# Kernel optimization log

Measured on AMD Instinct MI355X. Metric: run time of the kernel, lower is better.

## Reference

```python
import jax, jax.numpy as jnp
import numpy as np

HIDDEN = 1280
NUM_HEADS = 20
HEAD_DIM = HIDDEN // NUM_HEADS
B, S = 2, 2048


def setup_inputs() -> dict:
    key = jax.random.key(0)
    k1, k2, k3, k4, k5 = jax.random.split(key, 5)
    scale_in = 1.0 / np.sqrt(HIDDEN)
    return {
        "x": jax.random.normal(k1, (B, S, HIDDEN), dtype=jnp.float32),
        "w_attn": jax.random.normal(k2, (HIDDEN, 3 * HIDDEN), dtype=jnp.float32) * scale_in,
        "b_attn": jax.random.normal(k3, (3 * HIDDEN,), dtype=jnp.float32) * 0.02,
        "w_proj": jax.random.normal(k4, (HIDDEN, HIDDEN), dtype=jnp.float32) * scale_in,
        "b_proj": jax.random.normal(k5, (HIDDEN,), dtype=jnp.float32) * 0.02,
    }


def reference(x, w_attn, b_attn, w_proj, b_proj):
    b, s, _ = x.shape
    scale = 1.0 / np.sqrt(HEAD_DIM)
    qkv = x @ w_attn + b_attn                      # [B,S,3H]
    q, k, v = jnp.split(qkv, 3, axis=-1)

    def heads(t):  # [B,S,H] -> [B,nh,S,hd]
        return t.reshape(b, s, NUM_HEADS, HEAD_DIM).transpose(0, 2, 1, 3)

    q, k, v = heads(q), heads(k), heads(v)
    attn = jnp.einsum("bhqd,bhkd->bhqk", q, k) * scale
    causal = jnp.tril(jnp.ones((s, s), dtype=bool))
    attn = jnp.where(causal, attn, jnp.float32(-jnp.inf))
    attn = jax.nn.softmax(attn, axis=-1)           # dropout = identity (eval)
    out = jnp.einsum("bhqk,bhkd->bhqd", attn, v)
    out = out.transpose(0, 2, 1, 3).reshape(b, s, HIDDEN)
    return out @ w_proj + b_proj
```

## Files before the change

kernel.cpp:

```cpp
#include <hip/hip_runtime.h>

typedef unsigned short u16;
typedef __attribute__((ext_vector_type(8))) short bf16x8;
typedef __attribute__((ext_vector_type(4))) float f32x4;
typedef __attribute__((ext_vector_type(4))) unsigned short u16x4;

#define MFMA16 __builtin_amdgcn_mfma_f32_16x16x32_bf16

__device__ __forceinline__ u16 f2bf(float f) {
  unsigned int u = __float_as_uint(f);
  u += 0x7fff + ((u >> 16) & 1);
  return (u16)(u >> 16);
}

__device__ __forceinline__ float vexp2(float x) {
  float r; asm("v_exp_f32 %0, %1" : "=v"(r) : "v"(x)); return r;
}

template<int CTRL>
__device__ __forceinline__ float dppf(float v) {
  return __int_as_float(__builtin_amdgcn_update_dpp(0, __float_as_int(v), CTRL, 0xF, 0xF, true));
}
__device__ __forceinline__ float rowsum16(float v) {
  v += dppf<0xB1>(v);
  v += dppf<0x4E>(v);
  v += dppf<0x141>(v);
  v += dppf<0x140>(v);
  return v;
}

__device__ __forceinline__ void gload_lds16(const void* g, void* l) {
  __builtin_amdgcn_global_load_lds((__attribute__((address_space(1))) void*)g,
                                   (__attribute__((address_space(3))) void*)l,
                                   16, 0, 0);
}

__global__ void k_cast(const float* __restrict__ src, u16* __restrict__ dst, int n4) {
  int i = blockIdx.x * 256 + threadIdx.x;
  if (i >= n4) return;
  const float4 v = reinterpret_cast<const float4*>(src)[i];
  u16x4 o = {f2bf(v.x), f2bf(v.y), f2bf(v.z), f2bf(v.w)};
  reinterpret_cast<u16x4*>(dst)[i] = o;
}

__global__ void k_transpose_cast(const float* __restrict__ src, u16* __restrict__ dst,
                                 int R, int C) {
  __shared__ float tile[64][65];
  const int t = threadIdx.x;
  const int c0 = blockIdx.x * 64, r0 = blockIdx.y * 64;
#pragma unroll
  for (int i = 0; i < 16; ++i) {
    int e = i * 256 + t;
    int r = e >> 6, c = e & 63;
    tile[r][c] = src[(size_t)(r0 + r) * C + (c0 + c)];
  }
  __syncthreads();
#pragma unroll
  for (int i = 0; i < 16; ++i) {
    int e = i * 256 + t;
    int r = e >> 6, c = e & 63;
    dst[(size_t)(c0 + r) * R + (r0 + c)] = f2bf(tile[c][r]);
  }
}

__global__ __launch_bounds__(256, 2) void k_gemm_qkv(
    const u16* __restrict__ A, const u16* __restrict__ Bt,
    const float* __restrict__ bias,
    u16* __restrict__ qo, u16* __restrict__ ko, u16* __restrict__ vt) {
  constexpr int K = 1280;
  __shared__ u16 Alds[128 * 64];
  __shared__ u16 Blds[128 * 64];
  const int t = threadIdx.x;
  const int lane = t & 63, wave = t >> 6;
  const int wr = wave >> 1, wc = wave & 1;
  const int l15 = lane & 15, lhi = lane >> 4;
  const int m0 = blockIdx.x * 128, n0 = blockIdx.y * 128;

  f32x4 acc[4][4];
#pragma unroll
  for (int mi = 0; mi < 4; ++mi)
#pragma unroll
    for (int ni = 0; ni < 4; ++ni) acc[mi][ni] = f32x4{0.f, 0.f, 0.f, 0.f};

  const int srow = t >> 3;
  const int scol = (t & 7) * 8;
  const u16* Ag = A + (size_t)(m0 + srow) * K + scol;
  const u16* Bg = Bt + (size_t)(n0 + srow) * K + scol;
  char* Al = (char*)Alds + wave * 1024;
  char* Bl = (char*)Blds + wave * 1024;

  for (int k0 = 0; k0 < K; k0 += 64) {
    __syncthreads();
#pragma unroll
    for (int it = 0; it < 4; ++it) {
      gload_lds16(Ag + (it * 32) * K + k0, Al + it * 4096);
      gload_lds16(Bg + (it * 32) * K + k0, Bl + it * 4096);
    }
    asm volatile("s_waitcnt vmcnt(0)" ::: "memory");
    __syncthreads();
    const u16* Ab = Alds + (wr * 64 + l15) * 64 + lhi * 8;
    const u16* Bb = Blds + (wc * 64 + l15) * 64 + lhi * 8;
    bf16x8 af[4][2], bfv[4][2];
#pragma unroll
    for (int x = 0; x < 4; ++x) {
      af[x][0] = *(const bf16x8*)(Ab + x * 1024);
      af[x][1] = *(const bf16x8*)(Ab + x * 1024 + 32);
      bfv[x][0] = *(const bf16x8*)(Bb + x * 1024);
      bfv[x][1] = *(const bf16x8*)(Bb + x * 1024 + 32);
    }
#pragma unroll
    for (int mi = 0; mi < 4; ++mi)
#pragma unroll
      for (int ni = 0; ni < 4; ++ni) {
        acc[mi][ni] = MFMA16(af[mi][0], bfv[ni][0], acc[mi][ni], 0, 0, 0);
        acc[mi][ni] = MFMA16(af[mi][1], bfv[ni][1], acc[mi][ni], 0, 0, 0);
      }
  }

  const int which = n0 >= 2560 ? 2 : (n0 >= 1280 ? 1 : 0);
  const int bbq = m0 >> 11;
  const int sbase = (m0 & 2047) + wr * 64;
  if (which < 2) {
    u16* outp = which == 0 ? qo : ko;
#pragma unroll
    for (int ni = 0; ni < 4; ++ni) {
      const int n_abs = n0 + wc * 64 + ni * 16 + l15;
      const int nn = n_abs - which * 1280;
      const int h = nn >> 6, d = nn & 63;
      const float bv = bias[n_abs];
#pragma unroll
      for (int mi = 0; mi < 4; ++mi) {
#pragma unroll
        for (int i = 0; i < 4; ++i) {
          const int ss = sbase + mi * 16 + lhi * 4 + i;
          outp[(((size_t)(bbq * 20 + h) * 2048 + ss) << 6) + d] = f2bf(acc[mi][ni][i] + bv);
        }
      }
    }
  } else {
#pragma unroll
    for (int ni = 0; ni < 4; ++ni) {
      const int n_abs = n0 + wc * 64 + ni * 16 + l15;
      const int nn = n_abs - 2560;
      const int h = nn >> 6, d = nn & 63;
      const float bv = bias[n_abs];
      u16* vrow = vt + ((size_t)(bbq * 20 + h) * 64 + d) * 2048;
#pragma unroll
      for (int mi = 0; mi < 4; ++mi) {
        const int ss = sbase + mi * 16 + lhi * 4;
        u16x4 pk = {f2bf(acc[mi][ni][0] + bv), f2bf(acc[mi][ni][1] + bv),
                    f2bf(acc[mi][ni][2] + bv), f2bf(acc[mi][ni][3] + bv)};
        *(u16x4*)(vrow + ss) = pk;
      }
    }
  }
}

__global__ __launch_bounds__(256, 2) void k_gemm_proj(
    const u16* __restrict__ A, const u16* __restrict__ Bt,
    const float* __restrict__ bias, float* __restrict__ out) {
  constexpr int K = 1280;
  __shared__ u16 Alds[128 * 64];
  __shared__ u16 Blds[128 * 64];
  const int t = threadIdx.x;
  const int lane = t & 63, wave = t >> 6;
  const int wr = wave >> 1, wc = wave & 1;
  const int l15 = lane & 15, lhi = lane >> 4;
  const int m0 = blockIdx.x * 128, n0 = blockIdx.y * 128;

  f32x4 acc[4][4];
#pragma unroll
  for (int mi = 0; mi < 4; ++mi)
#pragma unroll
    for (int ni = 0; ni < 4; ++ni) acc[mi][ni] = f32x4{0.f, 0.f, 0.f, 0.f};

  const int srow = t >> 3;
  const int scol = (t & 7) * 8;
  const u16* Ag = A + (size_t)(m0 + srow) * K + scol;
  const u16* Bg = Bt + (size_t)(n0 + srow) * K + scol;
  char* Al = (char*)Alds + wave * 1024;
  char* Bl = (char*)Blds + wave * 1024;

  for (int k0 = 0; k0 < K; k0 += 64) {
    __syncthreads();
#pragma unroll
    for (int it = 0; it < 4; ++it) {
      gload_lds16(Ag + (it * 32) * K + k0, Al + it * 4096);
      gload_lds16(Bg + (it * 32) * K + k0, Bl + it * 4096);
    }
    asm volatile("s_waitcnt vmcnt(0)" ::: "memory");
    __syncthreads();
    const u16* Ab = Alds + (wr * 64 + l15) * 64 + lhi * 8;
    const u16* Bb = Blds + (wc * 64 + l15) * 64 + lhi * 8;
    bf16x8 af[4][2], bfv[4][2];
#pragma unroll
    for (int x = 0; x < 4; ++x) {
      af[x][0] = *(const bf16x8*)(Ab + x * 1024);
      af[x][1] = *(const bf16x8*)(Ab + x * 1024 + 32);
      bfv[x][0] = *(const bf16x8*)(Bb + x * 1024);
      bfv[x][1] = *(const bf16x8*)(Bb + x * 1024 + 32);
    }
#pragma unroll
    for (int mi = 0; mi < 4; ++mi)
#pragma unroll
      for (int ni = 0; ni < 4; ++ni) {
        acc[mi][ni] = MFMA16(af[mi][0], bfv[ni][0], acc[mi][ni], 0, 0, 0);
        acc[mi][ni] = MFMA16(af[mi][1], bfv[ni][1], acc[mi][ni], 0, 0, 0);
      }
  }

#pragma unroll
  for (int ni = 0; ni < 4; ++ni) {
    const int n_abs = n0 + wc * 64 + ni * 16 + l15;
    const float bv = bias[n_abs];
#pragma unroll
    for (int mi = 0; mi < 4; ++mi) {
#pragma unroll
      for (int i = 0; i < 4; ++i) {
        const int m_abs = m0 + wr * 64 + mi * 16 + lhi * 4 + i;
        out[(size_t)m_abs * 1280 + n_abs] = acc[mi][ni][i] + bv;
      }
    }
  }
}

__global__ __launch_bounds__(256, 3) void k_attn11(
    const u16* __restrict__ Qg, const u16* __restrict__ Kg,
    const u16* __restrict__ VT, u16* __restrict__ ao) {
  __shared__ __align__(16) char kvs[2][16384];
  __shared__ u16 Plds[4][32 * 72];
  const int t = threadIdx.x;
  const int lane = t & 63, wave = t >> 6;
  const int l15 = lane & 15, lhi = lane >> 4;
  const int bh = blockIdx.x;
  const int qt = 15 - blockIdx.y;
  const int bb = bh / 20, hh = bh % 20;
  const int q0w = qt * 128 + wave * 32;
  const int nkv = 2 * (qt + 1);
  const size_t base = (size_t)bh * 2048 * 64;
  const size_t vtb = (size_t)bh * 64 * 2048;
  u16* Pw = Plds[wave];

  const int sls = (lane & 7) ^ (lane >> 3);
  const int soff0 = ((lhi ^ (lane & 7)) << 4);
  const int soff1 = (((4 + lhi) ^ (lane & 7)) << 4);

  bf16x8 qf[2][2];
#pragma unroll
  for (int mr = 0; mr < 2; ++mr)
#pragma unroll
    for (int kk = 0; kk < 2; ++kk)
      qf[mr][kk] = *(const bf16x8*)(Qg + base + (size_t)(q0w + mr * 16 + l15) * 64 + kk * 32 + lhi * 8);

  f32x4 o[2][4];
  float lp[2][4];
#pragma unroll
  for (int mr = 0; mr < 2; ++mr) {
#pragma unroll
    for (int i = 0; i < 4; ++i) lp[mr][i] = 0.f;
#pragma unroll
    for (int dc = 0; dc < 4; ++dc) o[mr][dc] = f32x4{0.f, 0.f, 0.f, 0.f};
  }
  const float c1 = 0.18033688f;
  const float M = 16.0f;
  const int lastw = (q0w + 31) >> 6;

  auto stage = [&](char* buf, int kv0) {
#pragma unroll
    for (int j = 0; j < 2; ++j) {
      const int r = j * 32 + wave * 8 + (lane >> 3);
      gload_lds16(Kg + base + (size_t)(kv0 + r) * 64 + sls * 8,
                  buf + j * 4096 + wave * 1024);
      gload_lds16(VT + vtb + (size_t)r * 2048 + kv0 + sls * 8,
                  buf + 8192 + j * 4096 + wave * 1024);
    }
  };

  stage(kvs[0], 0);

  for (int tk = 0; tk < nkv; ++tk) {
    const int kv0 = tk * 64;
    if (tk + 1 < nkv) {
      stage(kvs[(tk + 1) & 1], kv0 + 64);
      asm volatile("s_waitcnt vmcnt(4)" ::: "memory");
    } else {
      asm volatile("s_waitcnt vmcnt(0)" ::: "memory");
    }
    __syncthreads();

    if (tk <= lastw) {
      const char* Krow = kvs[tk & 1] + l15 * 128;
      const char* Vrow = kvs[tk & 1] + 8192 + l15 * 128;
      f32x4 sc[2][4];
#pragma unroll
      for (int c = 0; c < 4; ++c) {
        const bf16x8 kf0 = *(const bf16x8*)(Krow + c * 2048 + soff0);
        const bf16x8 kf1 = *(const bf16x8*)(Krow + c * 2048 + soff1);
#pragma unroll
        for (int mr = 0; mr < 2; ++mr) {
          f32x4 z = MFMA16(qf[mr][0], kf0, f32x4{0.f, 0.f, 0.f, 0.f}, 0, 0, 0);
          z = MFMA16(qf[mr][1], kf1, z, 0, 0, 0);
          sc[mr][c] = z;
        }
      }
      if (kv0 + 63 > q0w) {
#pragma unroll
        for (int mr = 0; mr < 2; ++mr)
#pragma unroll
          for (int c = 0; c < 4; ++c)
#pragma unroll
            for (int i = 0; i < 4; ++i) {
              const int qa = q0w + mr * 16 + lhi * 4 + i;
              const int ka = kv0 + c * 16 + l15;
              sc[mr][c][i] = (ka <= qa) ? sc[mr][c][i] : -3.0e38f;
            }
      }
#pragma unroll
      for (int mr = 0; mr < 2; ++mr)
#pragma unroll
        for (int i = 0; i < 4; ++i) {
          float psum = 0.f;
#pragma unroll
          for (int c = 0; c < 4; ++c) {
            const float p = vexp2(__builtin_fmaf(sc[mr][c][i], c1, -M));
            psum += p;
            Pw[(mr * 16 + lhi * 4 + i) * 72 + c * 16 + l15] = (u16)(__float_as_uint(p) >> 16);
          }
          lp[mr][i] += psum;
        }
      bf16x8 pf[2][2];
#pragma unroll
      for (int mr = 0; mr < 2; ++mr)
#pragma unroll
        for (int kk = 0; kk < 2; ++kk)
          pf[mr][kk] = *(const bf16x8*)&Pw[(mr * 16 + l15) * 72 + kk * 32 + lhi * 8];
#pragma unroll
      for (int dc = 0; dc < 4; ++dc) {
        const bf16x8 vf0 = *(const bf16x8*)(Vrow + dc * 2048 + soff0);
        const bf16x8 vf1 = *(const bf16x8*)(Vrow + dc * 2048 + soff1);
#pragma unroll
        for (int mr = 0; mr < 2; ++mr) {
          o[mr][dc] = MFMA16(pf[mr][0], vf0, o[mr][dc], 0, 0, 0);
          o[mr][dc] = MFMA16(pf[mr][1], vf1, o[mr][dc], 0, 0, 0);
        }
      }
    }
    __syncthreads();
  }

#pragma unroll
  for (int mr = 0; mr < 2; ++mr)
#pragma unroll
    for (int i = 0; i < 4; ++i) {
      const float lfull = rowsum16(lp[mr][i]);
      const float inv = 1.0f / lfull;
      const int qa = q0w + mr * 16 + lhi * 4 + i;
#pragma unroll
      for (int dc = 0; dc < 4; ++dc) {
        const int d = dc * 16 + l15;
        ao[((size_t)(bb * 2048 + qa)) * 1280 + hh * 64 + d] = f2bf(o[mr][dc][i] * inv);
      }
    }
}

extern "C" void kernel_launch(void* const* d_in, const int* in_sizes, int n_in,
                              void* d_out, int out_size, void* d_ws, size_t ws_size,
                              hipStream_t stream) {
  (void)in_sizes; (void)n_in; (void)out_size; (void)ws_size;
  const float* x      = (const float*)d_in[0];
  const float* w_attn = (const float*)d_in[1];
  const float* b_attn = (const float*)d_in[2];
  const float* w_proj = (const float*)d_in[3];
  const float* b_proj = (const float*)d_in[4];
  float* out = (float*)d_out;

  char* ws = (char*)d_ws;
  u16* x_bf = (u16*)(ws + 0);
  u16* wa_t = (u16*)(ws + 10485760);
  u16* wp_t = (u16*)(ws + 20316160);
  u16* q_ws = (u16*)(ws + 23592960);
  u16* k_ws = (u16*)(ws + 34078720);
  u16* vt   = (u16*)(ws + 44564480);
  u16* ao   = x_bf;

  k_cast<<<5120, 256, 0, stream>>>(x, x_bf, 4096 * 1280 / 4);
  k_transpose_cast<<<dim3(60, 20), 256, 0, stream>>>(w_attn, wa_t, 1280, 3840);
  k_transpose_cast<<<dim3(20, 20), 256, 0, stream>>>(w_proj, wp_t, 1280, 1280);
  k_gemm_qkv<<<dim3(32, 30), 256, 0, stream>>>(x_bf, wa_t, b_attn, q_ws, k_ws, vt);
  k_attn11<<<dim3(40, 16), 256, 0, stream>>>(q_ws, k_ws, vt, ao);
  k_gemm_proj<<<dim3(32, 10), 256, 0, stream>>>(ao, wp_t, b_proj, out);
}
```

Before: 147.4 us.

## Double-buffer LDS tiles in QKV and projection GEMMs to overlap loads with MFMA

Both GEMM kernels now keep two LDS buffers for the A and B tiles and issue the global-to-LDS loads for the next K step before computing on the current one. This aims to hide global load latency behind the MFMA work and drops one barrier per iteration. LDS use doubles to 64KB per block, which may cut the number of blocks that fit per CU under launch_bounds(256,2). The GEMMs are only part of the total time, since attention dominates.

```diff
diff --git a/kernel.cpp b/kernel.cpp
--- a/kernel.cpp
+++ b/kernel.cpp
@@ -68,8 +68,8 @@
     const float* __restrict__ bias,
     u16* __restrict__ qo, u16* __restrict__ ko, u16* __restrict__ vt) {
   constexpr int K = 1280;
-  __shared__ u16 Alds[128 * 64];
-  __shared__ u16 Blds[128 * 64];
+  __shared__ u16 Alds[2][128 * 64];
+  __shared__ u16 Blds[2][128 * 64];
   const int t = threadIdx.x;
   const int lane = t & 63, wave = t >> 6;
   const int wr = wave >> 1, wc = wave & 1;
@@ -86,20 +86,26 @@
   const int scol = (t & 7) * 8;
   const u16* Ag = A + (size_t)(m0 + srow) * K + scol;
   const u16* Bg = Bt + (size_t)(n0 + srow) * K + scol;
-  char* Al = (char*)Alds + wave * 1024;
-  char* Bl = (char*)Blds + wave * 1024;
-
-  for (int k0 = 0; k0 < K; k0 += 64) {
-    __syncthreads();
+
+  auto stage = [&](int buf, int k0) {
+    char* Al = (char*)Alds[buf] + wave * 1024;
+    char* Bl = (char*)Blds[buf] + wave * 1024;
 #pragma unroll
     for (int it = 0; it < 4; ++it) {
       gload_lds16(Ag + (it * 32) * K + k0, Al + it * 4096);
       gload_lds16(Bg + (it * 32) * K + k0, Bl + it * 4096);
     }
-    asm volatile("s_waitcnt vmcnt(0)" ::: "memory");
-    __syncthreads();
-    const u16* Ab = Alds + (wr * 64 + l15) * 64 + lhi * 8;
-    const u16* Bb = Blds + (wc * 64 + l15) * 64 + lhi * 8;
+  };
+
+  stage(0, 0);
+  asm volatile("s_waitcnt vmcnt(0)" ::: "memory");
+  __syncthreads();
+
+  int cur = 0;
+  for (int k0 = 0; k0 < K; k0 += 64) {
+    if (k0 + 64 < K) stage(cur ^ 1, k0 + 64);
+    const u16* Ab = Alds[cur] + (wr * 64 + l15) * 64 + lhi * 8;
+    const u16* Bb = Blds[cur] + (wc * 64 + l15) * 64 + lhi * 8;
     bf16x8 af[4][2], bfv[4][2];
 #pragma unroll
     for (int x = 0; x < 4; ++x) {
@@ -115,6 +121,9 @@
         acc[mi][ni] = MFMA16(af[mi][0], bfv[ni][0], acc[mi][ni], 0, 0, 0);
         acc[mi][ni] = MFMA16(af[mi][1], bfv[ni][1], acc[mi][ni], 0, 0, 0);
       }
+    asm volatile("s_waitcnt vmcnt(0)" ::: "memory");
+    __syncthreads();
+    cur ^= 1;
   }
 
   const int which = n0 >= 2560 ? 2 : (n0 >= 1280 ? 1 : 0);
@@ -160,8 +169,8 @@
     const u16* __restrict__ A, const u16* __restrict__ Bt,
     const float* __restrict__ bias, float* __restrict__ out) {
   constexpr int K = 1280;
-  __shared__ u16 Alds[128 * 64];
-  __shared__ u16 Blds[128 * 64];
+  __shared__ u16 Alds[2][128 * 64];
+  __shared__ u16 Blds[2][128 * 64];
   const int t = threadIdx.x;
   const int lane = t & 63, wave = t >> 6;
   const int wr = wave >> 1, wc = wave & 1;
@@ -178,20 +187,26 @@
   const int scol = (t & 7) * 8;
   const u16* Ag = A + (size_t)(m0 + srow) * K + scol;
   const u16* Bg = Bt + (size_t)(n0 + srow) * K + scol;
-  char* Al = (char*)Alds + wave * 1024;
-  char* Bl = (char*)Blds + wave * 1024;
-
-  for (int k0 = 0; k0 < K; k0 += 64) {
-    __syncthreads();
+
+  auto stage = [&](int buf, int k0) {
+    char* Al = (char*)Alds[buf] + wave * 1024;
+    char* Bl = (char*)Blds[buf] + wave * 1024;
 #pragma unroll
     for (int it = 0; it < 4; ++it) {
       gload_lds16(Ag + (it * 32) * K + k0, Al + it * 4096);
       gload_lds16(Bg + (it * 32) * K + k0, Bl + it * 4096);
     }
-    asm volatile("s_waitcnt vmcnt(0)" ::: "memory");
-    __syncthreads();
-    const u16* Ab = Alds + (wr * 64 + l15) * 64 + lhi * 8;
-    const u16* Bb = Blds + (wc * 64 + l15) * 64 + lhi * 8;
+  };
+
+  stage(0, 0);
+  asm volatile("s_waitcnt vmcnt(0)" ::: "memory");
+  __syncthreads();
+
+  int cur = 0;
+  for (int k0 = 0; k0 < K; k0 += 64) {
+    if (k0 + 64 < K) stage(cur ^ 1, k0 + 64);
+    const u16* Ab = Alds[cur] + (wr * 64 + l15) * 64 + lhi * 8;
+    const u16* Bb = Blds[cur] + (wc * 64 + l15) * 64 + lhi * 8;
     bf16x8 af[4][2], bfv[4][2];
 #pragma unroll
     for (int x = 0; x < 4; ++x) {
@@ -207,6 +222,9 @@
         acc[mi][ni] = MFMA16(af[mi][0], bfv[ni][0], acc[mi][ni], 0, 0, 0);
         acc[mi][ni] = MFMA16(af[mi][1], bfv[ni][1], acc[mi][ni], 0, 0, 0);
       }
+    asm volatile("s_waitcnt vmcnt(0)" ::: "memory");
+    __syncthreads();
+    cur ^= 1;
   }
 
 #pragma unroll
```

After: 162.2 us. 1.1x slower.

## Merge prep kernels into one launch and halve proj GEMM M-tile

Applied to the files above, without the earlier changes.

The cast of x and the two weight transpose-casts are folded into a single kernel whose block index selects the job, which removes two launches and their gaps. The projection GEMM tile shrinks from 128x128 to 64x128, doubling the grid to 640 blocks so more CUs are busy on the 256-CU device. In exchange, B-tile data is reused less per block and the global loads per MFMA rise.

```diff
diff --git a/kernel.cpp b/kernel.cpp
--- a/kernel.cpp
+++ b/kernel.cpp
@@ -35,19 +35,31 @@
                                    16, 0, 0);
 }
 
-__global__ void k_cast(const float* __restrict__ src, u16* __restrict__ dst, int n4) {
-  int i = blockIdx.x * 256 + threadIdx.x;
-  if (i >= n4) return;
-  const float4 v = reinterpret_cast<const float4*>(src)[i];
-  u16x4 o = {f2bf(v.x), f2bf(v.y), f2bf(v.z), f2bf(v.w)};
-  reinterpret_cast<u16x4*>(dst)[i] = o;
-}
-
-__global__ void k_transpose_cast(const float* __restrict__ src, u16* __restrict__ dst,
-                                 int R, int C) {
+__global__ void k_prep(const float* __restrict__ x, u16* __restrict__ x_bf,
+                       const float* __restrict__ w_attn, u16* __restrict__ wa_t,
+                       const float* __restrict__ w_proj, u16* __restrict__ wp_t) {
   __shared__ float tile[64][65];
+  const int blk = blockIdx.x;
   const int t = threadIdx.x;
-  const int c0 = blockIdx.x * 64, r0 = blockIdx.y * 64;
+  if (blk < 5120) {
+    const int i = blk * 256 + t;
+    const float4 v = reinterpret_cast<const float4*>(x)[i];
+    u16x4 o = {f2bf(v.x), f2bf(v.y), f2bf(v.z), f2bf(v.w)};
+    reinterpret_cast<u16x4*>(x_bf)[i] = o;
+    return;
+  }
+  const float* src;
+  u16* dst;
+  int R, C, c0, r0;
+  if (blk < 6320) {
+    const int id = blk - 5120;
+    src = w_attn; dst = wa_t; R = 1280; C = 3840;
+    c0 = (id % 60) * 64; r0 = (id / 60) * 64;
+  } else {
+    const int id = blk - 6320;
+    src = w_proj; dst = wp_t; R = 1280; C = 1280;
+    c0 = (id % 20) * 64; r0 = (id / 20) * 64;
+  }
 #pragma unroll
   for (int i = 0; i < 16; ++i) {
     int e = i * 256 + t;
@@ -160,17 +172,17 @@
     const u16* __restrict__ A, const u16* __restrict__ Bt,
     const float* __restrict__ bias, float* __restrict__ out) {
   constexpr int K = 1280;
-  __shared__ u16 Alds[128 * 64];
+  __shared__ u16 Alds[64 * 64];
   __shared__ u16 Blds[128 * 64];
   const int t = threadIdx.x;
   const int lane = t & 63, wave = t >> 6;
   const int wr = wave >> 1, wc = wave & 1;
   const int l15 = lane & 15, lhi = lane >> 4;
-  const int m0 = blockIdx.x * 128, n0 = blockIdx.y * 128;
-
-  f32x4 acc[4][4];
-#pragma unroll
-  for (int mi = 0; mi < 4; ++mi)
+  const int m0 = blockIdx.x * 64, n0 = blockIdx.y * 128;
+
+  f32x4 acc[2][4];
+#pragma unroll
+  for (int mi = 0; mi < 2; ++mi)
 #pragma unroll
     for (int ni = 0; ni < 4; ++ni) acc[mi][ni] = f32x4{0.f, 0.f, 0.f, 0.f};
 
@@ -184,24 +196,28 @@
   for (int k0 = 0; k0 < K; k0 += 64) {
     __syncthreads();
 #pragma unroll
-    for (int it = 0; it < 4; ++it) {
+    for (int it = 0; it < 2; ++it)
       gload_lds16(Ag + (it * 32) * K + k0, Al + it * 4096);
+#pragma unroll
+    for (int it = 0; it < 4; ++it)
       gload_lds16(Bg + (it * 32) * K + k0, Bl + it * 4096);
-    }
     asm volatile("s_waitcnt vmcnt(0)" ::: "memory");
     __syncthreads();
-    const u16* Ab = Alds + (wr * 64 + l15) * 64 + lhi * 8;
+    const u16* Ab = Alds + (wr * 32 + l15) * 64 + lhi * 8;
     const u16* Bb = Blds + (wc * 64 + l15) * 64 + lhi * 8;
-    bf16x8 af[4][2], bfv[4][2];
-#pragma unroll
-    for (int x = 0; x < 4; ++x) {
+    bf16x8 af[2][2], bfv[4][2];
+#pragma unroll
+    for (int x = 0; x < 2; ++x) {
       af[x][0] = *(const bf16x8*)(Ab + x * 1024);
       af[x][1] = *(const bf16x8*)(Ab + x * 1024 + 32);
+    }
+#pragma unroll
+    for (int x = 0; x < 4; ++x) {
       bfv[x][0] = *(const bf16x8*)(Bb + x * 1024);
       bfv[x][1] = *(const bf16x8*)(Bb + x * 1024 + 32);
     }
 #pragma unroll
-    for (int mi = 0; mi < 4; ++mi)
+    for (int mi = 0; mi < 2; ++mi)
 #pragma unroll
       for (int ni = 0; ni < 4; ++ni) {
         acc[mi][ni] = MFMA16(af[mi][0], bfv[ni][0], acc[mi][ni], 0, 0, 0);
@@ -214,10 +230,10 @@
     const int n_abs = n0 + wc * 64 + ni * 16 + l15;
     const float bv = bias[n_abs];
 #pragma unroll
-    for (int mi = 0; mi < 4; ++mi) {
+    for (int mi = 0; mi < 2; ++mi) {
 #pragma unroll
       for (int i = 0; i < 4; ++i) {
-        const int m_abs = m0 + wr * 64 + mi * 16 + lhi * 4 + i;
+        const int m_abs = m0 + wr * 32 + mi * 16 + lhi * 4 + i;
         out[(size_t)m_abs * 1280 + n_abs] = acc[mi][ni][i] + bv;
       }
     }
@@ -383,10 +399,8 @@
   u16* vt   = (u16*)(ws + 44564480);
   u16* ao   = x_bf;
 
-  k_cast<<<5120, 256, 0, stream>>>(x, x_bf, 4096 * 1280 / 4);
-  k_transpose_cast<<<dim3(60, 20), 256, 0, stream>>>(w_attn, wa_t, 1280, 3840);
-  k_transpose_cast<<<dim3(20, 20), 256, 0, stream>>>(w_proj, wp_t, 1280, 1280);
+  k_prep<<<6720, 256, 0, stream>>>(x, x_bf, w_attn, wa_t, w_proj, wp_t);
   k_gemm_qkv<<<dim3(32, 30), 256, 0, stream>>>(x_bf, wa_t, b_attn, q_ws, k_ws, vt);
   k_attn11<<<dim3(40, 16), 256, 0, stream>>>(q_ws, k_ws, vt, ao);
-  k_gemm_proj<<<dim3(32, 10), 256, 0, stream>>>(ao, wp_t, b_proj, out);
-}
+  k_gemm_proj<<<dim3(64, 10), 256, 0, stream>>>(ao, wp_t, b_proj, out);
+}
```

Result: faster. 137.8 us, median of 2 (-6.5%).
